# Kernel optimization log

Measured on AMD Instinct MI355X. Metric: run time of the kernel, lower is better.

## Reference

```python
import jax, jax.numpy as jnp
import numpy as np

DDD = (0.83, 0.68, 0.54, 0.41, 0.29, 0.18, 0.09, 0.0)  # SONNET decile thresholds
NUM_INSTANCES = 16  # fixed label budget: mask values in 0..NUM_INSTANCES (0 = background)


def setup_inputs() -> dict:
    key = jax.random.key(0)
    k1, k2, k3 = jax.random.split(key, 3)
    B, C, W, H = 2, 8, 128, 128
    pred = jax.random.normal(k1, (B, C, W, H), dtype=jnp.float32)
    mask = jax.random.randint(k2, (B, W, H), 0, NUM_INSTANCES + 1, dtype=jnp.int32)
    ignored_map = jax.random.uniform(k3, (B, W, H), dtype=jnp.float32)
    return {"pred": pred, "mask": mask, "ignored_map": ignored_map}


def _edt(nuclei):
    """Exact Euclidean distance transform of boolean masks, vectorized over [B,K].
    nuclei: bool [B,K,W,H]. Returns float32 [B,K,W,H]: distance from each True
    pixel to the nearest False pixel (0 on False pixels), matching
    scipy.ndimage.distance_transform_edt via the separable squared-EDT identity
    D2[i,j] = min_{j'} ( G2[i,j'] + (j-j')^2 ),  G2[i,j] = min_{i': bg[i',j]} (i-i')^2.
    """
    bg = ~nuclei
    B, K, W, H = nuclei.shape
    INF = jnp.float32(1e9)
    di = jnp.arange(W, dtype=jnp.float32)
    d2i = (di[:, None] - di[None, :]) ** 2  # [W, W'] squared row offsets
    # G2[b,k,i,j] = min over i' (background rows) of (i - i')^2   -> [B,K,W,H]
    G2 = jnp.min(jnp.where(bg[:, :, None, :, :], d2i[None, None, :, :, None], INF), axis=3)
    dj = jnp.arange(H, dtype=jnp.float32)
    d2j = (dj[:, None] - dj[None, :]) ** 2  # [H, H'] squared column offsets
    # D2[b,k,i,j] = min over j' of G2[b,k,i,j'] + (j - j')^2
    D2 = jnp.min(G2[:, :, :, None, :] + d2j[None, None, None, :, :], axis=4)
    return jnp.sqrt(D2)


def _build_gt_sonnet(mask):
    """mask: int [B,W,H] instance labels (0 = background) -> gt_sonnet float32 [B,8,W,H]."""
    labels = jnp.arange(1, NUM_INSTANCES + 1, dtype=mask.dtype)
    nuclei = mask[:, None, :, :] == labels[None, :, None, None]  # [B,K,W,H]
    d = _edt(nuclei)
    # per-instance normalization: norm(img) = img / max(img) if max != 0
    m = jnp.max(d, axis=(2, 3), keepdims=True)
    d = jnp.where(m > 0, d / jnp.where(m > 0, m, 1.0), d)
    # thresholding: <0.5 -> 0, then >0.7 -> 1
    d = jnp.where(d < 0.5, 0.0, d)
    d = jnp.where(d > 0.7, 1.0, d)
    ddd = jnp.asarray(DDD, dtype=jnp.float32)  # [8] lower bin edges
    hi = jnp.concatenate([jnp.asarray([jnp.inf], dtype=jnp.float32), ddd[:-1]])  # upper edges (i==0 unbounded)
    de = d[:, :, None, :, :]  # [B,K,1,W,H]
    bins = (de >= ddd[None, None, :, None, None]) & (de < hi[None, None, :, None, None])
    # restricting to nuclei matches the original for all bins (bin 0 needs d>=0.83>0,
    # and background pixels have d==0, so they never enter bin 0 anyway)
    bins = bins & nuclei[:, :, None, :, :]
    return jnp.sum(bins.astype(jnp.float32), axis=1)  # [B,8,W,H]


def reference(pred, mask, ignored_map):
    gt_sonnet = _build_gt_sonnet(mask)
    diff = pred - gt_sonnet
    ad = jnp.abs(diff)
    l1 = jnp.where(ad < 1.0, 0.5 * diff * diff, ad - 0.5)  # SmoothL1, beta=1
    offset_loss = jnp.mean(jnp.mean(l1, axis=1) * ignored_map)
    return offset_loss, gt_sonnet
```

## Files before the change

kernel.cpp:

```cpp
#include <hip/hip_runtime.h>

#define KK 16
#define NPIX 16384


__global__ __launch_bounds__(256) void edt_kernel(const int* __restrict__ mask,
                                                  int* __restrict__ maxpart,
                                                  float* __restrict__ acc,
                                                  unsigned int* __restrict__ cnt,
                                                  unsigned short* __restrict__ d2) {
    __shared__ alignas(16) unsigned char  nuc[NPIX];
    __shared__ alignas(16) unsigned short sdn[NPIX];
    __shared__ alignas(16) unsigned short sup[NPIX];
    __shared__ int wmax[4];

    const int bid = blockIdx.x;
    const int t   = threadIdx.x;
    const int b1  = bid >> 7;
    const int k1  = (bid >> 3) & 15;
    const int rg  = bid & 7;

    if (bid == 0 && t == 0) { *acc = 0.0f; *cnt = 0u; }

    const int label = k1 + 1;
    const int4* m4 = (const int4*)(mask + b1 * NPIX);
    #pragma unroll
    for (int it = 0; it < 16; ++it) {
        const int idx = t + 256 * it;
        const int4 v = m4[idx];
        uchar4 u;
        u.x = (v.x == label); u.y = (v.y == label);
        u.z = (v.z == label); u.w = (v.w == label);
        *(uchar4*)&nuc[idx * 4] = u;
    }
    __syncthreads();

    if (t < 128) {
        const int j = t;
        int dist = 200;
        #pragma unroll 4
        for (int i = 0; i < 128; ++i) {
            dist = nuc[i * 128 + j] ? min(dist + 1, 200) : 0;
            sdn[i * 128 + j] = (unsigned short)dist;
        }
    } else {
        const int j = t - 128;
        int dist = 200;
        #pragma unroll 4
        for (int i = 127; i >= 0; --i) {
            dist = nuc[i * 128 + j] ? min(dist + 1, 200) : 0;
            sup[i * 128 + j] = (unsigned short)dist;
        }
    }
    __syncthreads();

    #pragma unroll
    for (int it = 0; it < 64; ++it) {
        const int idx = t + 256 * it;
        const int nd = min((int)sdn[idx], (int)sup[idx]);
        sdn[idx] = (unsigned short)(nd * nd);
    }
    __syncthreads();

    const int row = rg * 16 + (t >> 4);
    const int c0  = (t & 15) * 8;
    const unsigned short* grow = &sdn[row * 128];

    const uint4 gv = *(const uint4*)(grow + c0);
    int g[8];
    g[0] = (int)(gv.x & 0xffffu); g[1] = (int)(gv.x >> 16);
    g[2] = (int)(gv.y & 0xffffu); g[3] = (int)(gv.y >> 16);
    g[4] = (int)(gv.z & 0xffffu); g[5] = (int)(gv.z >> 16);
    g[6] = (int)(gv.w & 0xffffu); g[7] = (int)(gv.w >> 16);

    int best[8];
    #pragma unroll
    for (int u = 0; u < 8; ++u) best[u] = 0x7fffffff;
    #pragma unroll
    for (int w = 0; w < 8; ++w) {
        #pragma unroll
        for (int u = 0; u < 8; ++u) {
            const int dj = u - w;
            best[u] = min(best[u], g[w] + dj * dj);
        }
    }
    int mb = 0;
    #pragma unroll
    for (int u = 0; u < 8; ++u) mb = max(mb, best[u]);

    for (int e = 0; e < 128; ++e) {
        if (!__any((e + 1) * (e + 1) < mb)) break;
        const int jl = c0 - 1 - e;
        const int jr = c0 + 8 + e;
        if (jl >= 0) {
            const int gl = (int)grow[jl];
            #pragma unroll
            for (int u = 0; u < 8; ++u) {
                const int dj = u + 1 + e;
                best[u] = min(best[u], gl + dj * dj);
            }
        }
        if (jr < 128) {
            const int gr = (int)grow[jr];
            #pragma unroll
            for (int u = 0; u < 8; ++u) {
                const int dj = 8 + e - u;
                best[u] = min(best[u], gr + dj * dj);
            }
        }
        mb = 0;
        #pragma unroll
        for (int u = 0; u < 8; ++u) mb = max(mb, best[u]);
    }

    uint4 w;
    w.x = (unsigned)best[0] | ((unsigned)best[1] << 16);
    w.y = (unsigned)best[2] | ((unsigned)best[3] << 16);
    w.z = (unsigned)best[4] | ((unsigned)best[5] << 16);
    w.w = (unsigned)best[6] | ((unsigned)best[7] << 16);
    *(uint4*)(d2 + (b1 * KK + k1) * NPIX + row * 128 + c0) = w;

    int bm = mb;
    #pragma unroll
    for (int off = 32; off; off >>= 1) bm = max(bm, __shfl_down(bm, off, 64));
    if ((t & 63) == 0) wmax[t >> 6] = bm;
    __syncthreads();
    if (t == 0)
        maxpart[bid] = max(max(wmax[0], wmax[1]), max(wmax[2], wmax[3]));
}

__global__ __launch_bounds__(128) void gt_loss_kernel(const float* __restrict__ pred,
                                                      const float* __restrict__ ign,
                                                      const int* __restrict__ mask,
                                                      const unsigned short* __restrict__ d2,
                                                      const int* __restrict__ maxpart,
                                                      float* __restrict__ out,
                                                      float* __restrict__ acc,
                                                      unsigned int* __restrict__ cnt) {
    __shared__ float msq[KK];
    __shared__ float wred[2];

    const int bid = blockIdx.x;
    const int t   = threadIdx.x;
    const int p   = bid * 128 + t;
    const int b   = bid >> 7;
    const int pp  = p & (NPIX - 1);

    if (t < KK) {
        const int base = b * 128 + t * 8;
        int mt = 0;
        #pragma unroll
        for (int r = 0; r < 8; ++r) mt = max(mt, maxpart[base + r]);
        msq[t] = __fsqrt_rn((float)mt);
    }
    __syncthreads();

    const int label = mask[p];
    int cbin = -1;
    if (label > 0) {
        const int k = label - 1;
        const float d  = __fsqrt_rn((float)d2[(b * KK + k) * NPIX + pp]);
        float dn = __fdiv_rn(d, msq[k]);
        if (dn < 0.5f) dn = 0.0f;
        if (dn > 0.7f) dn = 1.0f;
        const float ddd[8] = {0.83f, 0.68f, 0.54f, 0.41f, 0.29f, 0.18f, 0.09f, 0.0f};
        #pragma unroll
        for (int c = 0; c < 8; ++c) {
            if (cbin < 0 && dn >= ddd[c]) cbin = c;
        }
    }

    float lsum = 0.0f;
    #pragma unroll
    for (int c = 0; c < 8; ++c) {
        const float g = (c == cbin) ? 1.0f : 0.0f;
        out[1 + (b * 8 + c) * NPIX + pp] = g;
        const float diff = pred[(b * 8 + c) * NPIX + pp] - g;
        const float ad = fabsf(diff);
        lsum += (ad < 1.0f) ? 0.5f * diff * diff : (ad - 0.5f);
    }
    float contrib = lsum * 0.125f * ign[p];

    #pragma unroll
    for (int off = 32; off; off >>= 1) contrib += __shfl_down(contrib, off, 64);
    if ((t & 63) == 0) wred[t >> 6] = contrib;
    __syncthreads();

    if (t == 0) {
        atomicAdd(acc, wred[0] + wred[1]);
        __threadfence();
        const unsigned int old = atomicAdd(cnt, 1u);
        if (old == 255u) {
            const float total = atomicAdd(acc, 0.0f);
            out[0] = total * (1.0f / 32768.0f);
        }
    }
}

extern "C" void kernel_launch(void* const* d_in, const int* in_sizes, int n_in,
                              void* d_out, int out_size, void* d_ws, size_t ws_size,
                              hipStream_t stream) {
    const float* pred = (const float*)d_in[0];
    const int*   mask = (const int*)d_in[1];
    const float* ign  = (const float*)d_in[2];
    float* out = (float*)d_out;

    int*            maxpart = (int*)d_ws;
    float*          acc     = (float*)((char*)d_ws + 1024);
    unsigned int*   cnt     = (unsigned int*)((char*)d_ws + 1028);
    unsigned short* d2      = (unsigned short*)((char*)d_ws + 4096);

    edt_kernel<<<256, 256, 0, stream>>>(mask, maxpart, acc, cnt, d2);
    gt_loss_kernel<<<256, 128, 0, stream>>>(pred, ign, mask, d2, maxpart, out, acc, cnt);
}
```

Measured before the change: 75.09 us.

## Fuse EDT and loss kernels into one cooperative launch with grid sync

After: 123.2 us. 64.1% more time.

```diff
diff --git a/kernel.cpp b/kernel.cpp
--- a/kernel.cpp
+++ b/kernel.cpp
@@ -1,18 +1,32 @@
 #include <hip/hip_runtime.h>
+#include <hip/hip_cooperative_groups.h>
+
+namespace cg = cooperative_groups;
 
 #define KK 16
 #define NPIX 16384
 
 
-__global__ __launch_bounds__(256) void edt_kernel(const int* __restrict__ mask,
-                                                  int* __restrict__ maxpart,
-                                                  float* __restrict__ acc,
-                                                  unsigned int* __restrict__ cnt,
-                                                  unsigned short* __restrict__ d2) {
+__device__ __forceinline__ unsigned pk_min_sq(unsigned a, unsigned b) {
+    const unsigned lo = min(a & 0xffffu, b & 0xffffu);
+    const unsigned hi = min(a >> 16, b >> 16);
+    return (lo * lo) | ((hi * hi) << 16);
+}
+
+__global__ __launch_bounds__(256) void fused_kernel(const int* __restrict__ mask,
+                                                    const float* __restrict__ pred,
+                                                    const float* __restrict__ ign,
+                                                    int* __restrict__ maxpart,
+                                                    float* __restrict__ acc,
+                                                    unsigned int* __restrict__ cnt,
+                                                    unsigned short* __restrict__ d2,
+                                                    float* __restrict__ out) {
     __shared__ alignas(16) unsigned char  nuc[NPIX];
     __shared__ alignas(16) unsigned short sdn[NPIX];
     __shared__ alignas(16) unsigned short sup[NPIX];
-    __shared__ int wmax[4];
+    __shared__ int   wmax[4];
+    __shared__ float msq[KK];
+    __shared__ float wred[4];
 
     const int bid = blockIdx.x;
     const int t   = threadIdx.x;
@@ -22,15 +36,16 @@
 
     if (bid == 0 && t == 0) { *acc = 0.0f; *cnt = 0u; }
 
-    const int label = k1 + 1;
+
+    const int label1 = k1 + 1;
     const int4* m4 = (const int4*)(mask + b1 * NPIX);
     #pragma unroll
     for (int it = 0; it < 16; ++it) {
         const int idx = t + 256 * it;
         const int4 v = m4[idx];
         uchar4 u;
-        u.x = (v.x == label); u.y = (v.y == label);
-        u.z = (v.z == label); u.w = (v.w == label);
+        u.x = (v.x == label1); u.y = (v.y == label1);
+        u.z = (v.z == label1); u.w = (v.w == label1);
         *(uchar4*)&nuc[idx * 4] = u;
     }
     __syncthreads();
@@ -54,11 +69,22 @@
     }
     __syncthreads();
 
-    #pragma unroll
-    for (int it = 0; it < 64; ++it) {
-        const int idx = t + 256 * it;
-        const int nd = min((int)sdn[idx], (int)sup[idx]);
-        sdn[idx] = (unsigned short)(nd * nd);
+    {
+        const uint4* a4 = (const uint4*)sdn;
+        const uint4* b4 = (const uint4*)sup;
+        uint4*       o4 = (uint4*)sdn;
+        #pragma unroll
+        for (int g = 0; g < 8; ++g) {
+            const int i4 = t + 256 * g;
+            const uint4 a = a4[i4];
+            const uint4 b = b4[i4];
+            uint4 r;
+            r.x = pk_min_sq(a.x, b.x);
+            r.y = pk_min_sq(a.y, b.y);
+            r.z = pk_min_sq(a.z, b.z);
+            r.w = pk_min_sq(a.w, b.w);
+            o4[i4] = r;
+        }
     }
     __syncthreads();
 
@@ -127,27 +153,17 @@
     __syncthreads();
     if (t == 0)
         maxpart[bid] = max(max(wmax[0], wmax[1]), max(wmax[2], wmax[3]));
-}
-
-__global__ __launch_bounds__(128) void gt_loss_kernel(const float* __restrict__ pred,
-                                                      const float* __restrict__ ign,
-                                                      const int* __restrict__ mask,
-                                                      const unsigned short* __restrict__ d2,
-                                                      const int* __restrict__ maxpart,
-                                                      float* __restrict__ out,
-                                                      float* __restrict__ acc,
-                                                      unsigned int* __restrict__ cnt) {
-    __shared__ float msq[KK];
-    __shared__ float wred[2];
-
-    const int bid = blockIdx.x;
-    const int t   = threadIdx.x;
-    const int p   = bid * 128 + t;
-    const int b   = bid >> 7;
+
+    __threadfence();
+    cg::this_grid().sync();
+
+    const int tp  = t & 127;
+    const int ch0 = (t >> 7) * 4;
+    const int p   = bid * 128 + tp;
     const int pp  = p & (NPIX - 1);
 
     if (t < KK) {
-        const int base = b * 128 + t * 8;
+        const int base = b1 * 128 + t * 8;
         int mt = 0;
         #pragma unroll
         for (int r = 0; r < 8; ++r) mt = max(mt, maxpart[base + r]);
@@ -159,7 +175,7 @@
     int cbin = -1;
     if (label > 0) {
         const int k = label - 1;
-        const float d  = __fsqrt_rn((float)d2[(b * KK + k) * NPIX + pp]);
+        const float d  = __fsqrt_rn((float)d2[(b1 * KK + k) * NPIX + pp]);
         float dn = __fdiv_rn(d, msq[k]);
         if (dn < 0.5f) dn = 0.0f;
         if (dn > 0.7f) dn = 1.0f;
@@ -172,10 +188,11 @@
 
     float lsum = 0.0f;
     #pragma unroll
-    for (int c = 0; c < 8; ++c) {
-        const float g = (c == cbin) ? 1.0f : 0.0f;
-        out[1 + (b * 8 + c) * NPIX + pp] = g;
-        const float diff = pred[(b * 8 + c) * NPIX + pp] - g;
+    for (int cc = 0; cc < 4; ++cc) {
+        const int c = ch0 + cc;
+        const float gt = (c == cbin) ? 1.0f : 0.0f;
+        out[1 + (b1 * 8 + c) * NPIX + pp] = gt;
+        const float diff = pred[(b1 * 8 + c) * NPIX + pp] - gt;
         const float ad = fabsf(diff);
         lsum += (ad < 1.0f) ? 0.5f * diff * diff : (ad - 0.5f);
     }
@@ -187,7 +204,7 @@
     __syncthreads();
 
     if (t == 0) {
-        atomicAdd(acc, wred[0] + wred[1]);
+        atomicAdd(acc, (wred[0] + wred[1]) + (wred[2] + wred[3]));
         __threadfence();
         const unsigned int old = atomicAdd(cnt, 1u);
         if (old == 255u) {
@@ -200,8 +217,8 @@
 extern "C" void kernel_launch(void* const* d_in, const int* in_sizes, int n_in,
                               void* d_out, int out_size, void* d_ws, size_t ws_size,
                               hipStream_t stream) {
+    const int*   mask = (const int*)d_in[1];
     const float* pred = (const float*)d_in[0];
-    const int*   mask = (const int*)d_in[1];
     const float* ign  = (const float*)d_in[2];
     float* out = (float*)d_out;
 
@@ -210,6 +227,8 @@
     unsigned int*   cnt     = (unsigned int*)((char*)d_ws + 1028);
     unsigned short* d2      = (unsigned short*)((char*)d_ws + 4096);
 
-    edt_kernel<<<256, 256, 0, stream>>>(mask, maxpart, acc, cnt, d2);
-    gt_loss_kernel<<<256, 128, 0, stream>>>(pred, ign, mask, d2, maxpart, out, acc, cnt);
+    void* args[] = {(void*)&mask, (void*)&pred, (void*)&ign, (void*)&maxpart,
+                    (void*)&acc, (void*)&cnt, (void*)&d2, (void*)&out};
+    hipLaunchCooperativeKernel((const void*)fused_kernel, dim3(256), dim3(256),
+                               args, 0, stream);
 }
```

## Scan mask directly from global and fuse min-square into row EDT pass

Applied to the files above, without the earlier changes.

New measurement: 74.10 us. No clear change (-1.3%).

```diff
diff --git a/kernel.cpp b/kernel.cpp
--- a/kernel.cpp
+++ b/kernel.cpp
@@ -9,7 +9,6 @@
                                                   float* __restrict__ acc,
                                                   unsigned int* __restrict__ cnt,
                                                   unsigned short* __restrict__ d2) {
-    __shared__ alignas(16) unsigned char  nuc[NPIX];
     __shared__ alignas(16) unsigned short sdn[NPIX];
     __shared__ alignas(16) unsigned short sup[NPIX];
     __shared__ int wmax[4];
@@ -22,56 +21,46 @@
 
     if (bid == 0 && t == 0) { *acc = 0.0f; *cnt = 0u; }
 
-    const int label = k1 + 1;
-    const int4* m4 = (const int4*)(mask + b1 * NPIX);
-    #pragma unroll
-    for (int it = 0; it < 16; ++it) {
-        const int idx = t + 256 * it;
-        const int4 v = m4[idx];
-        uchar4 u;
-        u.x = (v.x == label); u.y = (v.y == label);
-        u.z = (v.z == label); u.w = (v.w == label);
-        *(uchar4*)&nuc[idx * 4] = u;
-    }
-    __syncthreads();
-
+    const int label1 = k1 + 1;
+    const int* mb = mask + b1 * NPIX;
     if (t < 128) {
         const int j = t;
         int dist = 200;
-        #pragma unroll 4
+        #pragma unroll 8
         for (int i = 0; i < 128; ++i) {
-            dist = nuc[i * 128 + j] ? min(dist + 1, 200) : 0;
+            dist = (mb[i * 128 + j] == label1) ? min(dist + 1, 200) : 0;
             sdn[i * 128 + j] = (unsigned short)dist;
         }
     } else {
         const int j = t - 128;
         int dist = 200;
-        #pragma unroll 4
+        #pragma unroll 8
         for (int i = 127; i >= 0; --i) {
-            dist = nuc[i * 128 + j] ? min(dist + 1, 200) : 0;
+            dist = (mb[i * 128 + j] == label1) ? min(dist + 1, 200) : 0;
             sup[i * 128 + j] = (unsigned short)dist;
         }
-    }
-    __syncthreads();
-
-    #pragma unroll
-    for (int it = 0; it < 64; ++it) {
-        const int idx = t + 256 * it;
-        const int nd = min((int)sdn[idx], (int)sup[idx]);
-        sdn[idx] = (unsigned short)(nd * nd);
     }
     __syncthreads();
 
     const int row = rg * 16 + (t >> 4);
     const int c0  = (t & 15) * 8;
-    const unsigned short* grow = &sdn[row * 128];
-
-    const uint4 gv = *(const uint4*)(grow + c0);
+    const unsigned short* ga = &sdn[row * 128];
+    const unsigned short* gb = &sup[row * 128];
+
+    const uint4 va = *(const uint4*)(ga + c0);
+    const uint4 vb = *(const uint4*)(gb + c0);
     int g[8];
-    g[0] = (int)(gv.x & 0xffffu); g[1] = (int)(gv.x >> 16);
-    g[2] = (int)(gv.y & 0xffffu); g[3] = (int)(gv.y >> 16);
-    g[4] = (int)(gv.z & 0xffffu); g[5] = (int)(gv.z >> 16);
-    g[6] = (int)(gv.w & 0xffffu); g[7] = (int)(gv.w >> 16);
+    {
+        const unsigned aw[4] = {va.x, va.y, va.z, va.w};
+        const unsigned bw[4] = {vb.x, vb.y, vb.z, vb.w};
+        #pragma unroll
+        for (int q = 0; q < 4; ++q) {
+            const int lo = min((int)(aw[q] & 0xffffu), (int)(bw[q] & 0xffffu));
+            const int hi = min((int)(aw[q] >> 16),     (int)(bw[q] >> 16));
+            g[2 * q]     = lo * lo;
+            g[2 * q + 1] = hi * hi;
+        }
+    }
 
     int best[8];
     #pragma unroll
@@ -84,16 +73,17 @@
             best[u] = min(best[u], g[w] + dj * dj);
         }
     }
-    int mb = 0;
-    #pragma unroll
-    for (int u = 0; u < 8; ++u) mb = max(mb, best[u]);
+    int mbst = 0;
+    #pragma unroll
+    for (int u = 0; u < 8; ++u) mbst = max(mbst, best[u]);
 
     for (int e = 0; e < 128; ++e) {
-        if (!__any((e + 1) * (e + 1) < mb)) break;
+        if (!__any((e + 1) * (e + 1) < mbst)) break;
         const int jl = c0 - 1 - e;
         const int jr = c0 + 8 + e;
         if (jl >= 0) {
-            const int gl = (int)grow[jl];
+            const int ndl = min((int)ga[jl], (int)gb[jl]);
+            const int gl  = ndl * ndl;
             #pragma unroll
             for (int u = 0; u < 8; ++u) {
                 const int dj = u + 1 + e;
@@ -101,16 +91,17 @@
             }
         }
         if (jr < 128) {
-            const int gr = (int)grow[jr];
+            const int ndr = min((int)ga[jr], (int)gb[jr]);
+            const int gr  = ndr * ndr;
             #pragma unroll
             for (int u = 0; u < 8; ++u) {
                 const int dj = 8 + e - u;
                 best[u] = min(best[u], gr + dj * dj);
             }
         }
-        mb = 0;
-        #pragma unroll
-        for (int u = 0; u < 8; ++u) mb = max(mb, best[u]);
+        mbst = 0;
+        #pragma unroll
+        for (int u = 0; u < 8; ++u) mbst = max(mbst, best[u]);
     }
 
     uint4 w;
@@ -120,7 +111,7 @@
     w.w = (unsigned)best[6] | ((unsigned)best[7] << 16);
     *(uint4*)(d2 + (b1 * KK + k1) * NPIX + row * 128 + c0) = w;
 
-    int bm = mb;
+    int bm = mbst;
     #pragma unroll
     for (int off = 32; off; off >>= 1) bm = max(bm, __shfl_down(bm, off, 64));
     if ((t & 63) == 0) wmax[t >> 6] = bm;
```
